# Kernel tuning notes

Hardware: AMD Instinct MI355X
Metric: run time of the kernel (lower is better)

The kernel has to match this reference:

```python
import jax, jax.numpy as jnp
import numpy as np

IN_FEATURES = 4096
OUT_FEATURES = 768
N_BITS = 8
SCALE = float(2 ** N_BITS - 1)  # 255
REG_WEIGHT = 0.001


def setup_inputs() -> dict:
    key = jax.random.key(0)
    k1, k2, k3 = jax.random.split(key, 3)
    latent = jax.random.normal(k1, (1024, IN_FEATURES), dtype=jnp.float32)
    true_sum = jax.random.uniform(k2, (1024, OUT_FEATURES * N_BITS), dtype=jnp.float32)
    # nn.init.uniform_(weight, -0.1, 0.1)
    weight = jax.random.uniform(k3, (IN_FEATURES, OUT_FEATURES * N_BITS),
                                dtype=jnp.float32, minval=-0.1, maxval=0.1)
    return {"latent": latent, "true_sum": true_sum, "weight": weight}


def _powers():
    # [1, 2, 4, ..., 2^(n-1)] with the top (sign) bit negated -> two's complement
    p = 2.0 ** jnp.arange(N_BITS, dtype=jnp.float32)
    return p.at[-1].multiply(-1.0)


def reference(latent, true_sum, weight):
    prob_weights = jax.nn.sigmoid(weight)                      # [in, out*n_bits]
    # min(|p-0|, |p-1|) = min(p, 1-p) for p in (0,1)
    reg_loss = REG_WEIGHT * jnp.minimum(prob_weights, 1.0 - prob_weights).mean()

    powers = _powers()                                         # [n_bits]
    int_weights = jnp.einsum('iob,b->io',
                             prob_weights.reshape(IN_FEATURES, -1, N_BITS),
                             powers)                           # [in, out]
    int_sum = jnp.einsum('nob,b->no',
                         true_sum.reshape(true_sum.shape[0], -1, N_BITS),
                         powers)                               # [B, out]

    # (latent[:, :, None] * int_weights[None]).sum(-2) == latent @ int_weights
    pred = jnp.einsum('bi,io->bo', latent, int_weights)        # [B, out]

    recon_loss = jnp.mean((pred / SCALE - int_sum / SCALE) ** 2)
    return (recon_loss + reg_loss, recon_loss, reg_loss)
```

## Files before the change

kernel.cpp:

```cpp
#include <hip/hip_runtime.h>
#include <hip/hip_bf16.h>
#include <stdint.h>

#define IN_F   4096
#define OUT_F  768
#define OUTB   (OUT_F * 8)
#define BATCH  1024
#define SPLITK 4
#define KSPAN  (IN_F / SPLITK)
#define BK     64
#define NIT    (KSPAN / BK)
#define PLANE  (BATCH * OUT_F)
#define PLANE4 (PLANE / 4)
#define EPIBLK 768

typedef short short8  __attribute__((ext_vector_type(8)));
typedef float f32x4   __attribute__((ext_vector_type(4)));
typedef unsigned int u32;

#define WS_WP    12582912
#define WS_LABF  18874368
#define WS_REGP  27262976
#define WS_SQP   27269120

__device__ __forceinline__ ushort f2bf(float f) {
    uint32_t u = __builtin_bit_cast(uint32_t, f);
    u += 0x7FFFu + ((u >> 16) & 1u);
    return (ushort)(u >> 16);
}

__device__ __forceinline__ float waveReduceSum(float v) {
    #pragma unroll
    for (int off = 32; off > 0; off >>= 1) v += __shfl_down(v, off, 64);
    return v;
}

__device__ __forceinline__ void glds16(const void* g, void* l) {
    __builtin_amdgcn_global_load_lds(
        (const __attribute__((address_space(1))) u32*)g,
        (__attribute__((address_space(3))) u32*)l, 16, 0, 0);
}

__global__ __launch_bounds__(256) void k_weights(const float* __restrict__ w,
                                                 const float* __restrict__ latent,
                                                 ushort* __restrict__ wp,
                                                 ushort* __restrict__ labf,
                                                 float* __restrict__ regpart) {
    if (blockIdx.x >= 1536) {
        int t = (blockIdx.x - 1536) * 256 + threadIdx.x;
        const float4* src = (const float4*)latent;
        uint4* dst = (uint4*)labf;
        #pragma unroll
        for (int j = 0; j < 4; j++) {
            int o = j * 131072 + t;
            float4 a0 = src[2 * o];
            float4 a1 = src[2 * o + 1];
            union { ushort u[8]; uint4 v; } pk;
            pk.u[0] = f2bf(a0.x); pk.u[1] = f2bf(a0.y); pk.u[2] = f2bf(a0.z); pk.u[3] = f2bf(a0.w);
            pk.u[4] = f2bf(a1.x); pk.u[5] = f2bf(a1.y); pk.u[6] = f2bf(a1.z); pk.u[7] = f2bf(a1.w);
            dst[o] = pk.v;
        }
        return;
    }

    int t  = blockIdx.x * 256 + threadIdx.x;
    int o  = t % OUT_F;
    int i8 = t / OUT_F;
    const float* src = w + (size_t)(i8 * 8) * OUTB + (size_t)o * 8;

    const float P[8] = {1.f, 2.f, 4.f, 8.f, 16.f, 32.f, 64.f, -128.f};
    float regsum = 0.f;
    union { ushort u[8]; uint4 v; } pk;

    #pragma unroll
    for (int r = 0; r < 8; r++) {
        float4 a = *(const float4*)(src + (size_t)r * OUTB);
        float4 b = *(const float4*)(src + (size_t)r * OUTB + 4);
        float x[8] = {a.x, a.y, a.z, a.w, b.x, b.y, b.z, b.w};
        float iw = 0.f;
        #pragma unroll
        for (int j = 0; j < 8; j++) {
            float p = __builtin_amdgcn_rcpf(1.f + __expf(-x[j]));
            iw += p * P[j];
            regsum += fminf(p, 1.f - p);
        }
        pk.u[r] = f2bf(iw);
    }
    *(uint4*)(wp + ((size_t)i8 * OUT_F + o) * 8) = pk.v;

    float ws = waveReduceSum(regsum);
    __shared__ float red[4];
    int lane = threadIdx.x & 63, wv = threadIdx.x >> 6;
    if (lane == 0) red[wv] = ws;
    __syncthreads();
    if (threadIdx.x == 0) regpart[blockIdx.x] = red[0] + red[1] + red[2] + red[3];
}

__global__ __launch_bounds__(256) void k_gemm(const ushort* __restrict__ labf,
                                              const ushort* __restrict__ wp,
                                              float* __restrict__ predp) {
    __shared__ __align__(16) ushort lA[2][64 * 72];
    __shared__ __align__(16) ushort lB[2][8 * 1032];

    const int tid  = threadIdx.x;
    const int n0   = blockIdx.x * 64;
    const int m0   = blockIdx.y * 64;
    const int bz   = blockIdx.z;
    const int kbase = bz * KSPAN;
    const int kg0   = kbase >> 3;
    const int lane = tid & 63, w = tid >> 6;
    const int wm = w >> 1, wn = w & 1;
    const int quad = lane >> 4, l16 = lane & 15;

    f32x4 acc[2][2] = {{{0.f,0.f,0.f,0.f},{0.f,0.f,0.f,0.f}},
                       {{0.f,0.f,0.f,0.f},{0.f,0.f,0.f,0.f}}};

    const int ar = tid >> 2, ac = tid & 3;
    const ushort* aptr = labf + (size_t)(m0 + ar) * IN_F + kbase + ac * 16;
    const ushort* bbase = wp + ((size_t)kg0 * OUT_F + n0 + lane) * 8;

    int buf = 0;
    glds16(bbase + (size_t)(2 * w) * OUT_F * 8,     &lB[0][(2 * w) * 1032]);
    glds16(bbase + (size_t)(2 * w + 1) * OUT_F * 8, &lB[0][(2 * w + 1) * 1032]);
    {
        uint4 a0 = *(const uint4*)aptr;
        uint4 a1 = *(const uint4*)(aptr + 8);
        *(uint4*)&lA[0][ar * 72 + ac * 16]     = a0;
        *(uint4*)&lA[0][ar * 72 + ac * 16 + 8] = a1;
    }
    __syncthreads();

    for (int it = 0; it < NIT; ++it) {
        const int nxt = buf ^ 1;
        uint4 a0, a1;
        if (it + 1 < NIT) {
            const ushort* bp = bbase + (size_t)(it + 1) * 8 * OUT_F * 8;
            glds16(bp + (size_t)(2 * w) * OUT_F * 8,     &lB[nxt][(2 * w) * 1032]);
            glds16(bp + (size_t)(2 * w + 1) * OUT_F * 8, &lB[nxt][(2 * w + 1) * 1032]);
            a0 = *(const uint4*)(aptr + (it + 1) * BK);
            a1 = *(const uint4*)(aptr + (it + 1) * BK + 8);
        }
        #pragma unroll
        for (int s = 0; s < 2; ++s) {
            short8 af0 = *(short8*)&lA[buf][(wm * 32 + l16) * 72 + s * 32 + quad * 8];
            short8 af1 = *(short8*)&lA[buf][(wm * 32 + 16 + l16) * 72 + s * 32 + quad * 8];
            short8 bf0 = *(short8*)&lB[buf][(s * 4 + quad) * 1032 + (wn * 32 + l16) * 8];
            short8 bf1 = *(short8*)&lB[buf][(s * 4 + quad) * 1032 + (wn * 32 + 16 + l16) * 8];
            acc[0][0] = __builtin_amdgcn_mfma_f32_16x16x32_bf16(af0, bf0, acc[0][0], 0, 0, 0);
            acc[0][1] = __builtin_amdgcn_mfma_f32_16x16x32_bf16(af0, bf1, acc[0][1], 0, 0, 0);
            acc[1][0] = __builtin_amdgcn_mfma_f32_16x16x32_bf16(af1, bf0, acc[1][0], 0, 0, 0);
            acc[1][1] = __builtin_amdgcn_mfma_f32_16x16x32_bf16(af1, bf1, acc[1][1], 0, 0, 0);
        }
        if (it + 1 < NIT) {
            *(uint4*)&lA[nxt][ar * 72 + ac * 16]     = a0;
            *(uint4*)&lA[nxt][ar * 72 + ac * 16 + 8] = a1;
        }
        __syncthreads();
        buf = nxt;
    }

    float* plane = predp + (size_t)bz * PLANE;
    #pragma unroll
    for (int fm = 0; fm < 2; fm++)
    #pragma unroll
    for (int fn = 0; fn < 2; fn++)
    #pragma unroll
    for (int r = 0; r < 4; r++) {
        int m = m0 + wm * 32 + fm * 16 + quad * 4 + r;
        int n = n0 + wn * 32 + fn * 16 + l16;
        plane[(size_t)m * OUT_F + n] = acc[fm][fn][r];
    }
}

__global__ __launch_bounds__(256) void k_epi(const float* __restrict__ predp,
                                             const float* __restrict__ tsum,
                                             float* __restrict__ sqpart) {
    int g = blockIdx.x * 256 + threadIdx.x;
    int m = g / (OUT_F / 4);
    int c = g % (OUT_F / 4);
    const float4* pp = (const float4*)predp;
    float4 p0 = pp[g];
    float4 p1 = pp[g + PLANE4];
    float4 p2 = pp[g + 2 * PLANE4];
    float4 p3 = pp[g + 3 * PLANE4];
    float pv[4] = {p0.x + p1.x + p2.x + p3.x, p0.y + p1.y + p2.y + p3.y,
                   p0.z + p1.z + p2.z + p3.z, p0.w + p1.w + p2.w + p3.w};
    const float* ts = tsum + (size_t)m * OUTB + (size_t)c * 32;
    float lsum = 0.f;
    #pragma unroll
    for (int j = 0; j < 4; j++) {
        float4 t0 = *(const float4*)(ts + j * 8);
        float4 t1 = *(const float4*)(ts + j * 8 + 4);
        float isum = t0.x + 2.f * t0.y + 4.f * t0.z + 8.f * t0.w
                   + 16.f * t1.x + 32.f * t1.y + 64.f * t1.z - 128.f * t1.w;
        float d = pv[j] - isum;
        lsum += d * d;
    }
    float wsum = waveReduceSum(lsum);
    __shared__ float red[4];
    if ((threadIdx.x & 63) == 0) red[threadIdx.x >> 6] = wsum;
    __syncthreads();
    if (threadIdx.x == 0)
        sqpart[blockIdx.x] = red[0] + red[1] + red[2] + red[3];
}

__global__ __launch_bounds__(256) void k_fin(const float* __restrict__ regpart,
                                             const float* __restrict__ sqpart,
                                             float* __restrict__ out) {
    int tid = threadIdx.x;
    float r = 0.f, s = 0.f;
    #pragma unroll
    for (int j = 0; j < 6; j++) r += regpart[tid + j * 256];
    #pragma unroll
    for (int j = 0; j < 3; j++) s += sqpart[tid + j * 256];
    r = waveReduceSum(r);
    s = waveReduceSum(s);
    __shared__ float redR[4], redS[4];
    int lane = tid & 63, wv = tid >> 6;
    if (lane == 0) { redR[wv] = r; redS[wv] = s; }
    __syncthreads();
    if (tid == 0) {
        float R = redR[0] + redR[1] + redR[2] + redR[3];
        float S = redS[0] + redS[1] + redS[2] + redS[3];
        float recon = S / ((float)(BATCH * OUT_F) * 255.f * 255.f);
        float reg   = 0.001f * R / (float)((size_t)IN_F * OUTB);
        out[0] = recon + reg;
        out[1] = recon;
        out[2] = reg;
    }
}

extern "C" void kernel_launch(void* const* d_in, const int* in_sizes, int n_in,
                              void* d_out, int out_size, void* d_ws, size_t ws_size,
                              hipStream_t stream) {
    const float* latent = (const float*)d_in[0];
    const float* tsum   = (const float*)d_in[1];
    const float* weight = (const float*)d_in[2];
    float* out      = (float*)d_out;
    float* predp    = (float*)d_ws;
    ushort* wp      = (ushort*)((char*)d_ws + WS_WP);
    ushort* labf    = (ushort*)((char*)d_ws + WS_LABF);
    float* regpart  = (float*)((char*)d_ws + WS_REGP);
    float* sqpart   = (float*)((char*)d_ws + WS_SQP);

    k_weights<<<2048, 256, 0, stream>>>(weight, latent, wp, labf, regpart);
    k_gemm<<<dim3(OUT_F / 64, BATCH / 64, SPLITK), 256, 0, stream>>>(labf, wp, predp);
    k_epi<<<EPIBLK, 256, 0, stream>>>(predp, tsum, sqpart);
    k_fin<<<1, 256, 0, stream>>>(regpart, sqpart, out);
}
```

Baseline: 201.7 us.

## Fold final reduction into epilogue via last-block atomics and remap GEMM grid to XCDs

Removes the separate single-block finalize kernel by having each epilogue block atomically accumulate its squared-error sum and increment a counter, so the last block computes the outputs. The GEMM launch becomes a 1D grid whose block index is decoded so that blocks sharing a split-K slice land on the same XCD, improving L2 locality for the shared weight and activation tiles. This trades one kernel launch for atomic contention and makes the float summation order nondeterministic.

```diff
diff --git a/kernel.cpp b/kernel.cpp
--- a/kernel.cpp
+++ b/kernel.cpp
@@ -13,15 +13,16 @@
 #define PLANE  (BATCH * OUT_F)
 #define PLANE4 (PLANE / 4)
 #define EPIBLK 768
+#define GEMMBLK 768
+
+#define WS_WP    12582912
+#define WS_LABF  18874368
+#define WS_REGP  27262976
+#define WS_CTRL  27269120
 
 typedef short short8  __attribute__((ext_vector_type(8)));
 typedef float f32x4   __attribute__((ext_vector_type(4)));
 typedef unsigned int u32;
-
-#define WS_WP    12582912
-#define WS_LABF  18874368
-#define WS_REGP  27262976
-#define WS_SQP   27269120
 
 __device__ __forceinline__ ushort f2bf(float f) {
     uint32_t u = __builtin_bit_cast(uint32_t, f);
@@ -45,7 +46,12 @@
                                                  const float* __restrict__ latent,
                                                  ushort* __restrict__ wp,
                                                  ushort* __restrict__ labf,
-                                                 float* __restrict__ regpart) {
+                                                 float* __restrict__ regpart,
+                                                 float* __restrict__ ctrl) {
+    if (blockIdx.x == 0 && threadIdx.x == 0) {
+        ctrl[0] = 0.f;
+        ((u32*)ctrl)[1] = 0u;
+    }
     if (blockIdx.x >= 1536) {
         int t = (blockIdx.x - 1536) * 256 + threadIdx.x;
         const float4* src = (const float4*)latent;
@@ -103,9 +109,12 @@
     __shared__ __align__(16) ushort lB[2][8 * 1032];
 
     const int tid  = threadIdx.x;
-    const int n0   = blockIdx.x * 64;
-    const int m0   = blockIdx.y * 64;
-    const int bz   = blockIdx.z;
+    const int d  = blockIdx.x;
+    const int xc = d & 7, s = d >> 3;
+    const int bz = xc >> 1;
+    const int tt = s + 96 * (xc & 1);
+    const int n0 = (tt % 12) * 64;
+    const int m0 = (tt / 12) * 64;
     const int kbase = bz * KSPAN;
     const int kg0   = kbase >> 3;
     const int lane = tid & 63, w = tid >> 6;
@@ -141,11 +150,11 @@
             a1 = *(const uint4*)(aptr + (it + 1) * BK + 8);
         }
         #pragma unroll
-        for (int s = 0; s < 2; ++s) {
-            short8 af0 = *(short8*)&lA[buf][(wm * 32 + l16) * 72 + s * 32 + quad * 8];
-            short8 af1 = *(short8*)&lA[buf][(wm * 32 + 16 + l16) * 72 + s * 32 + quad * 8];
-            short8 bf0 = *(short8*)&lB[buf][(s * 4 + quad) * 1032 + (wn * 32 + l16) * 8];
-            short8 bf1 = *(short8*)&lB[buf][(s * 4 + quad) * 1032 + (wn * 32 + 16 + l16) * 8];
+        for (int ss = 0; ss < 2; ++ss) {
+            short8 af0 = *(short8*)&lA[buf][(wm * 32 + l16) * 72 + ss * 32 + quad * 8];
+            short8 af1 = *(short8*)&lA[buf][(wm * 32 + 16 + l16) * 72 + ss * 32 + quad * 8];
+            short8 bf0 = *(short8*)&lB[buf][(ss * 4 + quad) * 1032 + (wn * 32 + l16) * 8];
+            short8 bf1 = *(short8*)&lB[buf][(ss * 4 + quad) * 1032 + (wn * 32 + 16 + l16) * 8];
             acc[0][0] = __builtin_amdgcn_mfma_f32_16x16x32_bf16(af0, bf0, acc[0][0], 0, 0, 0);
             acc[0][1] = __builtin_amdgcn_mfma_f32_16x16x32_bf16(af0, bf1, acc[0][1], 0, 0, 0);
             acc[1][0] = __builtin_amdgcn_mfma_f32_16x16x32_bf16(af1, bf0, acc[1][0], 0, 0, 0);
@@ -174,7 +183,9 @@
 
 __global__ __launch_bounds__(256) void k_epi(const float* __restrict__ predp,
                                              const float* __restrict__ tsum,
-                                             float* __restrict__ sqpart) {
+                                             const float* __restrict__ regpart,
+                                             float* __restrict__ ctrl,
+                                             float* __restrict__ out) {
     int g = blockIdx.x * 256 + threadIdx.x;
     int m = g / (OUT_F / 4);
     int c = g % (OUT_F / 4);
@@ -198,30 +209,28 @@
     }
     float wsum = waveReduceSum(lsum);
     __shared__ float red[4];
-    if ((threadIdx.x & 63) == 0) red[threadIdx.x >> 6] = wsum;
-    __syncthreads();
-    if (threadIdx.x == 0)
-        sqpart[blockIdx.x] = red[0] + red[1] + red[2] + red[3];
-}
-
-__global__ __launch_bounds__(256) void k_fin(const float* __restrict__ regpart,
-                                             const float* __restrict__ sqpart,
-                                             float* __restrict__ out) {
-    int tid = threadIdx.x;
-    float r = 0.f, s = 0.f;
-    #pragma unroll
-    for (int j = 0; j < 6; j++) r += regpart[tid + j * 256];
-    #pragma unroll
-    for (int j = 0; j < 3; j++) s += sqpart[tid + j * 256];
+    __shared__ int lastf;
+    int lane = threadIdx.x & 63, wv = threadIdx.x >> 6;
+    if (lane == 0) red[wv] = wsum;
+    __syncthreads();
+    if (threadIdx.x == 0) {
+        atomicAdd(&ctrl[0], red[0] + red[1] + red[2] + red[3]);
+        u32 t = __hip_atomic_fetch_add((u32*)ctrl + 1, 1u,
+                                       __ATOMIC_RELEASE, __HIP_MEMORY_SCOPE_AGENT);
+        lastf = (t == (u32)(EPIBLK - 1));
+    }
+    __syncthreads();
+    if (!lastf) return;
+
+    float r = 0.f;
+    #pragma unroll
+    for (int j = 0; j < 6; j++) r += regpart[threadIdx.x + j * 256];
     r = waveReduceSum(r);
-    s = waveReduceSum(s);
-    __shared__ float redR[4], redS[4];
-    int lane = tid & 63, wv = tid >> 6;
-    if (lane == 0) { redR[wv] = r; redS[wv] = s; }
-    __syncthreads();
-    if (tid == 0) {
-        float R = redR[0] + redR[1] + redR[2] + redR[3];
-        float S = redS[0] + redS[1] + redS[2] + redS[3];
+    if (lane == 0) red[wv] = r;
+    __syncthreads();
+    if (threadIdx.x == 0) {
+        float S = atomicAdd(&ctrl[0], 0.0f);
+        float R = red[0] + red[1] + red[2] + red[3];
         float recon = S / ((float)(BATCH * OUT_F) * 255.f * 255.f);
         float reg   = 0.001f * R / (float)((size_t)IN_F * OUTB);
         out[0] = recon + reg;
@@ -241,10 +250,9 @@
     ushort* wp      = (ushort*)((char*)d_ws + WS_WP);
     ushort* labf    = (ushort*)((char*)d_ws + WS_LABF);
     float* regpart  = (float*)((char*)d_ws + WS_REGP);
-    float* sqpart   = (float*)((char*)d_ws + WS_SQP);
-
-    k_weights<<<2048, 256, 0, stream>>>(weight, latent, wp, labf, regpart);
-    k_gemm<<<dim3(OUT_F / 64, BATCH / 64, SPLITK), 256, 0, stream>>>(labf, wp, predp);
-    k_epi<<<EPIBLK, 256, 0, stream>>>(predp, tsum, sqpart);
-    k_fin<<<1, 256, 0, stream>>>(regpart, sqpart, out);
-}
+    float* ctrl     = (float*)((char*)d_ws + WS_CTRL);
+
+    k_weights<<<2048, 256, 0, stream>>>(weight, latent, wp, labf, regpart, ctrl);
+    k_gemm<<<GEMMBLK, 256, 0, stream>>>(labf, wp, predp);
+    k_epi<<<EPIBLK, 256, 0, stream>>>(predp, tsum, regpart, ctrl, out);
+}
```

Result: slower. 224.7 us (+11.4%).

## Triple-buffer GEMM tiles with direct-to-LDS loads and XOR swizzled A layout

Applied to the files above, without the earlier changes.

Restructures the split-K GEMM main loop into a three-stage LDS ring. Both A and B tiles are now loaded with global_load_lds, where A previously went through registers. Explicit vmcnt waits and a single barrier per iteration let loads for iteration it+2 overlap compute on iteration it. The A tile uses an XOR swizzle instead of row padding to avoid LDS bank conflicts. The cost is more shared memory per block and a hand-tuned waitcnt that depends on exactly four outstanding loads per stage.

```diff
diff --git a/kernel.cpp b/kernel.cpp
--- a/kernel.cpp
+++ b/kernel.cpp
@@ -14,14 +14,14 @@
 #define PLANE4 (PLANE / 4)
 #define EPIBLK 768
 
-typedef short short8  __attribute__((ext_vector_type(8)));
-typedef float f32x4   __attribute__((ext_vector_type(4)));
-typedef unsigned int u32;
-
 #define WS_WP    12582912
 #define WS_LABF  18874368
 #define WS_REGP  27262976
 #define WS_SQP   27269120
+
+typedef short short8  __attribute__((ext_vector_type(8)));
+typedef float f32x4   __attribute__((ext_vector_type(4)));
+typedef unsigned int u32;
 
 __device__ __forceinline__ ushort f2bf(float f) {
     uint32_t u = __builtin_bit_cast(uint32_t, f);
@@ -99,8 +99,8 @@
 __global__ __launch_bounds__(256) void k_gemm(const ushort* __restrict__ labf,
                                               const ushort* __restrict__ wp,
                                               float* __restrict__ predp) {
-    __shared__ __align__(16) ushort lA[2][64 * 72];
-    __shared__ __align__(16) ushort lB[2][8 * 1032];
+    __shared__ __align__(16) ushort lA3[3][64 * 64];
+    __shared__ __align__(16) ushort lB3[3][8 * 512];
 
     const int tid  = threadIdx.x;
     const int n0   = blockIdx.x * 64;
@@ -111,53 +111,70 @@
     const int lane = tid & 63, w = tid >> 6;
     const int wm = w >> 1, wn = w & 1;
     const int quad = lane >> 4, l16 = lane & 15;
+    const int xA = (l16 & 7) << 4;
 
     f32x4 acc[2][2] = {{{0.f,0.f,0.f,0.f},{0.f,0.f,0.f,0.f}},
                        {{0.f,0.f,0.f,0.f},{0.f,0.f,0.f,0.f}}};
 
-    const int ar = tid >> 2, ac = tid & 3;
-    const ushort* aptr = labf + (size_t)(m0 + ar) * IN_F + kbase + ac * 16;
-    const ushort* bbase = wp + ((size_t)kg0 * OUT_F + n0 + lane) * 8;
-
-    int buf = 0;
-    glds16(bbase + (size_t)(2 * w) * OUT_F * 8,     &lB[0][(2 * w) * 1032]);
-    glds16(bbase + (size_t)(2 * w + 1) * OUT_F * 8, &lB[0][(2 * w + 1) * 1032]);
-    {
-        uint4 a0 = *(const uint4*)aptr;
-        uint4 a1 = *(const uint4*)(aptr + 8);
-        *(uint4*)&lA[0][ar * 72 + ac * 16]     = a0;
-        *(uint4*)&lA[0][ar * 72 + ac * 16 + 8] = a1;
-    }
-    __syncthreads();
-
-    for (int it = 0; it < NIT; ++it) {
-        const int nxt = buf ^ 1;
-        uint4 a0, a1;
-        if (it + 1 < NIT) {
-            const ushort* bp = bbase + (size_t)(it + 1) * 8 * OUT_F * 8;
-            glds16(bp + (size_t)(2 * w) * OUT_F * 8,     &lB[nxt][(2 * w) * 1032]);
-            glds16(bp + (size_t)(2 * w + 1) * OUT_F * 8, &lB[nxt][(2 * w + 1) * 1032]);
-            a0 = *(const uint4*)(aptr + (it + 1) * BK);
-            a1 = *(const uint4*)(aptr + (it + 1) * BK + 8);
-        }
-        #pragma unroll
-        for (int s = 0; s < 2; ++s) {
-            short8 af0 = *(short8*)&lA[buf][(wm * 32 + l16) * 72 + s * 32 + quad * 8];
-            short8 af1 = *(short8*)&lA[buf][(wm * 32 + 16 + l16) * 72 + s * 32 + quad * 8];
-            short8 bf0 = *(short8*)&lB[buf][(s * 4 + quad) * 1032 + (wn * 32 + l16) * 8];
-            short8 bf1 = *(short8*)&lB[buf][(s * 4 + quad) * 1032 + (wn * 32 + 16 + l16) * 8];
-            acc[0][0] = __builtin_amdgcn_mfma_f32_16x16x32_bf16(af0, bf0, acc[0][0], 0, 0, 0);
-            acc[0][1] = __builtin_amdgcn_mfma_f32_16x16x32_bf16(af0, bf1, acc[0][1], 0, 0, 0);
-            acc[1][0] = __builtin_amdgcn_mfma_f32_16x16x32_bf16(af1, bf0, acc[1][0], 0, 0, 0);
-            acc[1][1] = __builtin_amdgcn_mfma_f32_16x16x32_bf16(af1, bf1, acc[1][1], 0, 0, 0);
-        }
-        if (it + 1 < NIT) {
-            *(uint4*)&lA[nxt][ar * 72 + ac * 16]     = a0;
-            *(uint4*)&lA[nxt][ar * 72 + ac * 16 + 8] = a1;
-        }
-        __syncthreads();
-        buf = nxt;
-    }
+    const int r8 = lane >> 3;
+    const int c8 = (lane & 7) ^ r8;
+    const int p0 = 2 * w, p1 = 2 * w + 1;
+    const ushort* aSrc0 = labf + (size_t)(m0 + 8 * p0 + r8) * IN_F + kbase + 8 * c8;
+    const ushort* aSrc1 = labf + (size_t)(m0 + 8 * p1 + r8) * IN_F + kbase + 8 * c8;
+    const ushort* bSrc0 = wp + ((size_t)(kg0 + p0) * OUT_F + n0 + lane) * 8;
+    const ushort* bSrc1 = wp + ((size_t)(kg0 + p1) * OUT_F + n0 + lane) * 8;
+
+    #define STAGE(bi, it_) do {                                                   \
+        glds16(aSrc0 + (size_t)(it_) * BK,              &lA3[bi][p0 * 512]);      \
+        glds16(aSrc1 + (size_t)(it_) * BK,              &lA3[bi][p1 * 512]);      \
+        glds16(bSrc0 + (size_t)(it_) * (8 * OUT_F * 8), &lB3[bi][p0 * 512]);      \
+        glds16(bSrc1 + (size_t)(it_) * (8 * OUT_F * 8), &lB3[bi][p1 * 512]);      \
+    } while (0)
+
+    #define MSTEP(bi) do {                                                        \
+        const char* Ab = (const char*)&lA3[bi][0];                                \
+        _Pragma("unroll")                                                         \
+        for (int ss = 0; ss < 2; ++ss) {                                          \
+            short8 af0 = *(const short8*)(Ab + ((wm * 32 + l16) << 7)             \
+                                             + ((ss * 64 + quad * 16) ^ xA));     \
+            short8 af1 = *(const short8*)(Ab + ((wm * 32 + 16 + l16) << 7)        \
+                                             + ((ss * 64 + quad * 16) ^ xA));     \
+            short8 bf0 = *(const short8*)&lB3[bi][(ss * 4 + quad) * 512           \
+                                                  + (wn * 32 + l16) * 8];         \
+            short8 bf1 = *(const short8*)&lB3[bi][(ss * 4 + quad) * 512           \
+                                                  + (wn * 32 + 16 + l16) * 8];    \
+            acc[0][0] = __builtin_amdgcn_mfma_f32_16x16x32_bf16(af0, bf0, acc[0][0], 0, 0, 0); \
+            acc[0][1] = __builtin_amdgcn_mfma_f32_16x16x32_bf16(af0, bf1, acc[0][1], 0, 0, 0); \
+            acc[1][0] = __builtin_amdgcn_mfma_f32_16x16x32_bf16(af1, bf0, acc[1][0], 0, 0, 0); \
+            acc[1][1] = __builtin_amdgcn_mfma_f32_16x16x32_bf16(af1, bf1, acc[1][1], 0, 0, 0); \
+        }                                                                         \
+    } while (0)
+
+    STAGE(0, 0);
+    STAGE(1, 1);
+    asm volatile("s_waitcnt vmcnt(4)" ::: "memory");
+    __builtin_amdgcn_s_barrier();
+    __builtin_amdgcn_sched_barrier(0);
+
+    int bR = 0, bW = 2;
+    for (int it = 0; it < NIT - 2; ++it) {
+        STAGE(bW, it + 2);
+        MSTEP(bR);
+        asm volatile("s_waitcnt vmcnt(4)" ::: "memory");
+        __builtin_amdgcn_s_barrier();
+        __builtin_amdgcn_sched_barrier(0);
+        bR = (bR + 1 == 3) ? 0 : bR + 1;
+        bW = (bW + 1 == 3) ? 0 : bW + 1;
+    }
+    MSTEP(bR);
+    asm volatile("s_waitcnt vmcnt(0)" ::: "memory");
+    __builtin_amdgcn_s_barrier();
+    __builtin_amdgcn_sched_barrier(0);
+    bR = (bR + 1 == 3) ? 0 : bR + 1;
+    MSTEP(bR);
+
+    #undef STAGE
+    #undef MSTEP
 
     float* plane = predp + (size_t)bz * PLANE;
     #pragma unroll
```

Result: no change. 199.0 us (-1.3%).

## Pre-pack GEMM operands into MFMA fragment layout and load straight to registers

Applied to the files above, without the earlier changes.

The prep kernel now writes latent and the bit-collapsed weights in a layout that already matches the MFMA fragment order, so each lane reads its 16-byte fragment with one coalesced global load. The GEMM drops LDS staging and block barriers entirely: each wave computes a 64x64 tile with a 4x4 accumulator grid and keeps four k-steps of fragments in flight in registers. The aim is to remove LDS traffic and syncs from the GEMM. In exchange, register pressure rises and A/B tiles are no longer shared between waves through LDS. Each wave re-reads its operands from global memory/L2, and the packing kernel's latent conversion now needs more blocks.

```diff
diff --git a/kernel.cpp b/kernel.cpp
--- a/kernel.cpp
+++ b/kernel.cpp
@@ -8,21 +8,21 @@
 #define BATCH  1024
 #define SPLITK 4
 #define KSPAN  (IN_F / SPLITK)
-#define BK     64
-#define NIT    (KSPAN / BK)
+#define NS     (KSPAN / 32)
 #define PLANE  (BATCH * OUT_F)
 #define PLANE4 (PLANE / 4)
 #define EPIBLK 768
 
-typedef short short8  __attribute__((ext_vector_type(8)));
-typedef float f32x4   __attribute__((ext_vector_type(4)));
-typedef unsigned int u32;
 
 #define WS_WP    12582912
 #define WS_LABF  18874368
 #define WS_REGP  27262976
 #define WS_SQP   27269120
 
+typedef short short8  __attribute__((ext_vector_type(8)));
+typedef float f32x4   __attribute__((ext_vector_type(4)));
+typedef unsigned int u32;
+
 __device__ __forceinline__ ushort f2bf(float f) {
     uint32_t u = __builtin_bit_cast(uint32_t, f);
     u += 0x7FFFu + ((u >> 16) & 1u);
@@ -35,31 +35,28 @@
     return v;
 }
 
-__device__ __forceinline__ void glds16(const void* g, void* l) {
-    __builtin_amdgcn_global_load_lds(
-        (const __attribute__((address_space(1))) u32*)g,
-        (__attribute__((address_space(3))) u32*)l, 16, 0, 0);
-}
-
 __global__ __launch_bounds__(256) void k_weights(const float* __restrict__ w,
                                                  const float* __restrict__ latent,
-                                                 ushort* __restrict__ wp,
-                                                 ushort* __restrict__ labf,
+                                                 uint4* __restrict__ bpk,
+                                                 uint4* __restrict__ apk,
                                                  float* __restrict__ regpart) {
     if (blockIdx.x >= 1536) {
-        int t = (blockIdx.x - 1536) * 256 + threadIdx.x;
-        const float4* src = (const float4*)latent;
-        uint4* dst = (uint4*)labf;
-        #pragma unroll
-        for (int j = 0; j < 4; j++) {
-            int o = j * 131072 + t;
-            float4 a0 = src[2 * o];
-            float4 a1 = src[2 * o + 1];
-            union { ushort u[8]; uint4 v; } pk;
-            pk.u[0] = f2bf(a0.x); pk.u[1] = f2bf(a0.y); pk.u[2] = f2bf(a0.z); pk.u[3] = f2bf(a0.w);
-            pk.u[4] = f2bf(a1.x); pk.u[5] = f2bf(a1.y); pk.u[6] = f2bf(a1.z); pk.u[7] = f2bf(a1.w);
-            dst[o] = pk.v;
-        }
+        int t2 = (blockIdx.x - 1536) * 256 + threadIdx.x;
+        int q  = t2 >> 4;
+        int kk = q & 255;
+        int mg = q >> 8;
+        int m  = (mg << 4) | (t2 & 15);
+        const float4* lrow = (const float4*)(latent + (size_t)m * IN_F + kk * 16);
+        float4 a0 = lrow[0], a1 = lrow[1], a2 = lrow[2], a3 = lrow[3];
+        union { ushort u[8]; uint4 v; } g1, g2;
+        g1.u[0]=f2bf(a0.x); g1.u[1]=f2bf(a0.y); g1.u[2]=f2bf(a0.z); g1.u[3]=f2bf(a0.w);
+        g1.u[4]=f2bf(a1.x); g1.u[5]=f2bf(a1.y); g1.u[6]=f2bf(a1.z); g1.u[7]=f2bf(a1.w);
+        g2.u[0]=f2bf(a2.x); g2.u[1]=f2bf(a2.y); g2.u[2]=f2bf(a2.z); g2.u[3]=f2bf(a2.w);
+        g2.u[4]=f2bf(a3.x); g2.u[5]=f2bf(a3.y); g2.u[6]=f2bf(a3.z); g2.u[7]=f2bf(a3.w);
+        uint4* dst = apk + (size_t)(mg * 128 + (kk >> 1)) * 64
+                         + (t2 & 15) + 32 * (kk & 1);
+        dst[0]  = g1.v;
+        dst[16] = g2.v;
         return;
     }
 
@@ -86,7 +83,7 @@
         }
         pk.u[r] = f2bf(iw);
     }
-    *(uint4*)(wp + ((size_t)i8 * OUT_F + o) * 8) = pk.v;
+    bpk[(size_t)((o >> 4) * 128 + (i8 >> 2)) * 64 + (o & 15) + ((i8 & 3) << 4)] = pk.v;
 
     float ws = waveReduceSum(regsum);
     __shared__ float red[4];
@@ -96,79 +93,63 @@
     if (threadIdx.x == 0) regpart[blockIdx.x] = red[0] + red[1] + red[2] + red[3];
 }
 
-__global__ __launch_bounds__(256) void k_gemm(const ushort* __restrict__ labf,
-                                              const ushort* __restrict__ wp,
+__global__ __launch_bounds__(128) void k_gemm(const uint4* __restrict__ apk,
+                                              const uint4* __restrict__ bpk,
                                               float* __restrict__ predp) {
-    __shared__ __align__(16) ushort lA[2][64 * 72];
-    __shared__ __align__(16) ushort lB[2][8 * 1032];
-
     const int tid  = threadIdx.x;
+    const int lane = tid & 63, w = tid >> 6;
     const int n0   = blockIdx.x * 64;
-    const int m0   = blockIdx.y * 64;
+    const int m0   = blockIdx.y * 128 + w * 64;
     const int bz   = blockIdx.z;
-    const int kbase = bz * KSPAN;
-    const int kg0   = kbase >> 3;
-    const int lane = tid & 63, w = tid >> 6;
-    const int wm = w >> 1, wn = w & 1;
+    const int kb32 = (bz * KSPAN) >> 5;
+
+    const uint4* Ag = apk + (size_t)((m0 >> 4) * 128 + kb32) * 64 + lane;
+    const uint4* Bg = bpk + (size_t)((n0 >> 4) * 128 + kb32) * 64 + lane;
+
+    f32x4 acc[4][4] = {};
+    uint4 af[4][4], bf[4][4];
+
+    #define ISSUE(SET, S) do {                                        \
+        _Pragma("unroll")                                             \
+        for (int i = 0; i < 4; ++i) {                                 \
+            af[SET][i] = Ag[i * 8192 + (S) * 64];                     \
+            bf[SET][i] = Bg[i * 8192 + (S) * 64];                     \
+        }                                                             \
+    } while (0)
+
+    #define MM(SET) do {                                              \
+        _Pragma("unroll")                                             \
+        for (int i = 0; i < 4; ++i)                                   \
+        _Pragma("unroll")                                             \
+        for (int j = 0; j < 4; ++j)                                   \
+            acc[i][j] = __builtin_amdgcn_mfma_f32_16x16x32_bf16(      \
+                __builtin_bit_cast(short8, af[SET][i]),               \
+                __builtin_bit_cast(short8, bf[SET][j]),               \
+                acc[i][j], 0, 0, 0);                                  \
+    } while (0)
+
+    ISSUE(0, 0); ISSUE(1, 1); ISSUE(2, 2); ISSUE(3, 3);
+    for (int s = 0; s < NS - 4; s += 4) {
+        MM(0); ISSUE(0, s + 4);
+        MM(1); ISSUE(1, s + 5);
+        MM(2); ISSUE(2, s + 6);
+        MM(3); ISSUE(3, s + 7);
+    }
+    MM(0); MM(1); MM(2); MM(3);
+    #undef ISSUE
+    #undef MM
+
     const int quad = lane >> 4, l16 = lane & 15;
-
-    f32x4 acc[2][2] = {{{0.f,0.f,0.f,0.f},{0.f,0.f,0.f,0.f}},
-                       {{0.f,0.f,0.f,0.f},{0.f,0.f,0.f,0.f}}};
-
-    const int ar = tid >> 2, ac = tid & 3;
-    const ushort* aptr = labf + (size_t)(m0 + ar) * IN_F + kbase + ac * 16;
-    const ushort* bbase = wp + ((size_t)kg0 * OUT_F + n0 + lane) * 8;
-
-    int buf = 0;
-    glds16(bbase + (size_t)(2 * w) * OUT_F * 8,     &lB[0][(2 * w) * 1032]);
-    glds16(bbase + (size_t)(2 * w + 1) * OUT_F * 8, &lB[0][(2 * w + 1) * 1032]);
-    {
-        uint4 a0 = *(const uint4*)aptr;
-        uint4 a1 = *(const uint4*)(aptr + 8);
-        *(uint4*)&lA[0][ar * 72 + ac * 16]     = a0;
-        *(uint4*)&lA[0][ar * 72 + ac * 16 + 8] = a1;
-    }
-    __syncthreads();
-
-    for (int it = 0; it < NIT; ++it) {
-        const int nxt = buf ^ 1;
-        uint4 a0, a1;
-        if (it + 1 < NIT) {
-            const ushort* bp = bbase + (size_t)(it + 1) * 8 * OUT_F * 8;
-            glds16(bp + (size_t)(2 * w) * OUT_F * 8,     &lB[nxt][(2 * w) * 1032]);
-            glds16(bp + (size_t)(2 * w + 1) * OUT_F * 8, &lB[nxt][(2 * w + 1) * 1032]);
-            a0 = *(const uint4*)(aptr + (it + 1) * BK);
-            a1 = *(const uint4*)(aptr + (it + 1) * BK + 8);
-        }
-        #pragma unroll
-        for (int s = 0; s < 2; ++s) {
-            short8 af0 = *(short8*)&lA[buf][(wm * 32 + l16) * 72 + s * 32 + quad * 8];
-            short8 af1 = *(short8*)&lA[buf][(wm * 32 + 16 + l16) * 72 + s * 32 + quad * 8];
-            short8 bf0 = *(short8*)&lB[buf][(s * 4 + quad) * 1032 + (wn * 32 + l16) * 8];
-            short8 bf1 = *(short8*)&lB[buf][(s * 4 + quad) * 1032 + (wn * 32 + 16 + l16) * 8];
-            acc[0][0] = __builtin_amdgcn_mfma_f32_16x16x32_bf16(af0, bf0, acc[0][0], 0, 0, 0);
-            acc[0][1] = __builtin_amdgcn_mfma_f32_16x16x32_bf16(af0, bf1, acc[0][1], 0, 0, 0);
-            acc[1][0] = __builtin_amdgcn_mfma_f32_16x16x32_bf16(af1, bf0, acc[1][0], 0, 0, 0);
-            acc[1][1] = __builtin_amdgcn_mfma_f32_16x16x32_bf16(af1, bf1, acc[1][1], 0, 0, 0);
-        }
-        if (it + 1 < NIT) {
-            *(uint4*)&lA[nxt][ar * 72 + ac * 16]     = a0;
-            *(uint4*)&lA[nxt][ar * 72 + ac * 16 + 8] = a1;
-        }
-        __syncthreads();
-        buf = nxt;
-    }
-
     float* plane = predp + (size_t)bz * PLANE;
     #pragma unroll
-    for (int fm = 0; fm < 2; fm++)
-    #pragma unroll
-    for (int fn = 0; fn < 2; fn++)
+    for (int i = 0; i < 4; i++)
+    #pragma unroll
+    for (int j = 0; j < 4; j++)
     #pragma unroll
     for (int r = 0; r < 4; r++) {
-        int m = m0 + wm * 32 + fm * 16 + quad * 4 + r;
-        int n = n0 + wn * 32 + fn * 16 + l16;
-        plane[(size_t)m * OUT_F + n] = acc[fm][fn][r];
+        int m = m0 + i * 16 + quad * 4 + r;
+        int n = n0 + j * 16 + l16;
+        plane[(size_t)m * OUT_F + n] = acc[i][j][r];
     }
 }
 
@@ -238,13 +219,13 @@
     const float* weight = (const float*)d_in[2];
     float* out      = (float*)d_out;
     float* predp    = (float*)d_ws;
-    ushort* wp      = (ushort*)((char*)d_ws + WS_WP);
-    ushort* labf    = (ushort*)((char*)d_ws + WS_LABF);
+    uint4* bpk      = (uint4*)((char*)d_ws + WS_WP);
+    uint4* apk      = (uint4*)((char*)d_ws + WS_LABF);
     float* regpart  = (float*)((char*)d_ws + WS_REGP);
     float* sqpart   = (float*)((char*)d_ws + WS_SQP);
 
-    k_weights<<<2048, 256, 0, stream>>>(weight, latent, wp, labf, regpart);
-    k_gemm<<<dim3(OUT_F / 64, BATCH / 64, SPLITK), 256, 0, stream>>>(labf, wp, predp);
+    k_weights<<<2560, 256, 0, stream>>>(weight, latent, bpk, apk, regpart);
+    k_gemm<<<dim3(OUT_F / 64, BATCH / 128, SPLITK), 128, 0, stream>>>(apk, bpk, predp);
     k_epi<<<EPIBLK, 256, 0, stream>>>(predp, tsum, sqpart);
     k_fin<<<1, 256, 0, stream>>>(regpart, sqpart, out);
 }
```

Measured after the change: 199.5 us. No clear change (-1.1%).
